# Performance work log

Measured on AMD Instinct MI355X. Metric: run time of the kernel, lower is better.

Reference implementation:

```python
import jax, jax.numpy as jnp
import numpy as np

N = 8192
E = 262144
D_IN = 256
D_OUT = 256
EPS = 1e-05


def setup_inputs() -> dict:
    key = jax.random.key(0)
    kx, ke0, ke1, kw = jax.random.split(key, 4)
    x = jax.random.normal(kx, (N, D_IN), dtype=jnp.float32)
    edge_index = jnp.stack([
        jax.random.randint(ke0, (E,), 0, N, dtype=jnp.int64),
        jax.random.randint(ke1, (E,), 0, N, dtype=jnp.int64),
    ], axis=0)
    # nn.Linear(in, out, bias=False): weight shape [out, in], kaiming-uniform-ish init
    bound = 1.0 / np.sqrt(D_IN)
    W = jax.random.uniform(kw, (D_OUT, D_IN), dtype=jnp.float32, minval=-bound, maxval=bound)
    return {"x": x, "edge_index": edge_index, "W": W}


def reference(x, edge_index, W):
    n = x.shape[0]
    # A_hat = I with edges set to 1 (set semantics; duplicates harmless)
    A_hat = jnp.eye(n, dtype=x.dtype).at[edge_index[0], edge_index[1]].set(1.0)
    # D_hat = diag(1/sqrt(rowsum + eps)); A_norm = D_hat @ A_hat @ D_hat
    d_inv = 1.0 / jnp.sqrt(A_hat.sum(axis=1) + EPS)  # [N]
    A_norm = d_inv[:, None] * A_hat * d_inv[None, :]  # [N, N]
    h = x @ W.T  # [N, D_OUT]
    return jax.nn.relu(A_norm @ h)
```

## Files before the change

kernel.cpp:

```cpp
#include <hip/hip_runtime.h>
#include <hip/hip_bf16.h>
#include <math.h>

#define N_NODES 8192
#define DIM 256
#define WPR 256
#define LSTRIDE 128

typedef __attribute__((ext_vector_type(8))) short bf16x8;
typedef __attribute__((ext_vector_type(4))) float f32x4;

__global__ __launch_bounds__(256) void init_all(const float* __restrict__ x,
                                                const float* __restrict__ W,
                                                unsigned* __restrict__ bitmap,
                                                __hip_bfloat16* __restrict__ xb,
                                                __hip_bfloat16* __restrict__ Wb) {
    unsigned tid = blockIdx.x * 256 + threadIdx.x;
    uint4 z = {0u, 0u, 0u, 0u};
    ((uint4*)bitmap)[tid] = z;
    const unsigned NX8 = N_NODES * DIM / 8;
    if (tid < NX8 + DIM * DIM / 8) {
        const float* src = x;
        __hip_bfloat16* dst = xb;
        size_t off = (size_t)tid * 8;
        if (tid >= NX8) { src = W; dst = Wb; off = (size_t)(tid - NX8) * 8; }
        float4 v0 = *(const float4*)(src + off);
        float4 v1 = *(const float4*)(src + off + 4);
        union { __hip_bfloat16 h[8]; uint4 u; } t;
        t.h[0] = __float2bfloat16(v0.x); t.h[1] = __float2bfloat16(v0.y);
        t.h[2] = __float2bfloat16(v0.z); t.h[3] = __float2bfloat16(v0.w);
        t.h[4] = __float2bfloat16(v1.x); t.h[5] = __float2bfloat16(v1.y);
        t.h[6] = __float2bfloat16(v1.z); t.h[7] = __float2bfloat16(v1.w);
        *(uint4*)(dst + off) = t.u;
    }
}

__global__ __launch_bounds__(256) void scatter_edges(const int* __restrict__ rows,
                                                     const int* __restrict__ cols,
                                                     unsigned* __restrict__ bitmap, int E) {
    int e = blockIdx.x * 256 + threadIdx.x;
    if (e >= E) return;
    int r = rows[e];
    int c = cols[e];
    atomicOr(&bitmap[(size_t)r * WPR + (c >> 5)], 1u << (c & 31));
}

__global__ __launch_bounds__(256) void dinv_and_list(const unsigned* __restrict__ bitmap,
                                                     float* __restrict__ dinv,
                                                     int* __restrict__ lens,
                                                     unsigned short* __restrict__ list) {
    int wave = threadIdx.x >> 6;
    int lane = threadIdx.x & 63;
    int row = blockIdx.x * 4 + wave;
    const uint4* base = (const uint4*)(bitmap + (size_t)row * WPR);
    uint4 w = base[lane];
    int c = __popc(w.x) + __popc(w.y) + __popc(w.z) + __popc(w.w);
    int dw = row >> 5;
    int diag = 0;
    if ((dw >> 2) == lane) {
        unsigned word = ((dw & 3) == 0) ? w.x : ((dw & 3) == 1) ? w.y : ((dw & 3) == 2) ? w.z : w.w;
        diag = (int)((word >> (row & 31)) & 1u);
    }
    unsigned long long db = __ballot(diag);
    int p = c;
#pragma unroll
    for (int off = 1; off < 64; off <<= 1) {
        int v = __shfl_up(p, off);
        if (lane >= off) p += v;
    }
    int total = __shfl(p, 63);
    unsigned short* lp = list + (size_t)row * LSTRIDE + (p - c);
    int k = 0;
    unsigned ws[4] = {w.x, w.y, w.z, w.w};
#pragma unroll
    for (int q = 0; q < 4; q++) {
        unsigned ww = ws[q];
        int bc = lane * 128 + q * 32;
        while (ww) {
            int b = __builtin_ctz(ww);
            ww &= ww - 1;
            lp[k++] = (unsigned short)(bc + b);
        }
    }
    int len = total + (db == 0ull ? 1 : 0);
    if (db == 0ull && lane == 0) list[(size_t)row * LSTRIDE + total] = (unsigned short)row;
    if (lane == 0) {
        lens[row] = len;
        dinv[row] = 1.0f / sqrtf((float)len + 1e-5f);
    }
}

__global__ __launch_bounds__(256) void gemm_mfma(const short* __restrict__ xb,
                                                 const short* __restrict__ Wb,
                                                 const float* __restrict__ dinv,
                                                 __hip_bfloat16* __restrict__ g) {
    int wave = threadIdx.x >> 6;
    int lane = threadIdx.x & 63;
    int bm = blockIdx.x * 64 + wave * 16;
    int bn = blockIdx.y * 64;
    int quad = lane >> 4;
    int l16 = lane & 15;
    f32x4 acc[4] = {};
    const short* arow = xb + (size_t)(bm + l16) * DIM + quad * 8;
#pragma unroll
    for (int k0 = 0; k0 < DIM; k0 += 32) {
        bf16x8 a = *(const bf16x8*)(arow + k0);
#pragma unroll
        for (int s = 0; s < 4; s++) {
            bf16x8 b = *(const bf16x8*)(Wb + (size_t)(bn + s * 16 + l16) * DIM + k0 + quad * 8);
            acc[s] = __builtin_amdgcn_mfma_f32_16x16x32_bf16(a, b, acc[s], 0, 0, 0);
        }
    }
#pragma unroll
    for (int r = 0; r < 4; r++) {
        int m = bm + quad * 4 + r;
        float s0 = dinv[m];
#pragma unroll
        for (int s = 0; s < 4; s++)
            g[(size_t)m * DIM + bn + s * 16 + l16] = __float2bfloat16(s0 * acc[s][r]);
    }
}

__global__ __launch_bounds__(128) void aggregate(const unsigned short* __restrict__ list,
                                                 const int* __restrict__ lens,
                                                 const uint4* __restrict__ g4,
                                                 const float* __restrict__ dinv,
                                                 float* __restrict__ out) {
    __shared__ unsigned short snbr[LSTRIDE];
    __shared__ float part[4][DIM];
    int row = blockIdx.x;
    int tid = threadIdx.x;
    snbr[tid] = list[(size_t)row * LSTRIDE + tid];
    int len = lens[row];
    __syncthreads();
    int gq = tid >> 5, l = tid & 31;
    float a0 = 0.f, a1 = 0.f, a2 = 0.f, a3 = 0.f, a4 = 0.f, a5 = 0.f, a6 = 0.f, a7 = 0.f;
    float b0 = 0.f, b1 = 0.f, b2 = 0.f, b3 = 0.f, b4 = 0.f, b5 = 0.f, b6 = 0.f, b7 = 0.f;
    int i = gq;
    for (; i + 4 < len; i += 8) {
        int n0 = snbr[i];
        int n1 = snbr[i + 4];
        uint4 u0 = g4[(size_t)n0 * 32 + l];
        uint4 u1 = g4[(size_t)n1 * 32 + l];
        a0 += __uint_as_float(u0.x << 16); a1 += __uint_as_float(u0.x & 0xffff0000u);
        a2 += __uint_as_float(u0.y << 16); a3 += __uint_as_float(u0.y & 0xffff0000u);
        a4 += __uint_as_float(u0.z << 16); a5 += __uint_as_float(u0.z & 0xffff0000u);
        a6 += __uint_as_float(u0.w << 16); a7 += __uint_as_float(u0.w & 0xffff0000u);
        b0 += __uint_as_float(u1.x << 16); b1 += __uint_as_float(u1.x & 0xffff0000u);
        b2 += __uint_as_float(u1.y << 16); b3 += __uint_as_float(u1.y & 0xffff0000u);
        b4 += __uint_as_float(u1.z << 16); b5 += __uint_as_float(u1.z & 0xffff0000u);
        b6 += __uint_as_float(u1.w << 16); b7 += __uint_as_float(u1.w & 0xffff0000u);
    }
    if (i < len) {
        int n0 = snbr[i];
        uint4 u0 = g4[(size_t)n0 * 32 + l];
        a0 += __uint_as_float(u0.x << 16); a1 += __uint_as_float(u0.x & 0xffff0000u);
        a2 += __uint_as_float(u0.y << 16); a3 += __uint_as_float(u0.y & 0xffff0000u);
        a4 += __uint_as_float(u0.z << 16); a5 += __uint_as_float(u0.z & 0xffff0000u);
        a6 += __uint_as_float(u0.w << 16); a7 += __uint_as_float(u0.w & 0xffff0000u);
    }
    float* pp = &part[gq][l * 8];
    pp[0] = a0 + b0; pp[1] = a1 + b1; pp[2] = a2 + b2; pp[3] = a3 + b3;
    pp[4] = a4 + b4; pp[5] = a5 + b5; pp[6] = a6 + b6; pp[7] = a7 + b7;
    __syncthreads();
    int f0 = tid * 2;
    float s = dinv[row];
    float r0 = (part[0][f0] + part[1][f0]) + (part[2][f0] + part[3][f0]);
    float r1 = (part[0][f0 + 1] + part[1][f0 + 1]) + (part[2][f0 + 1] + part[3][f0 + 1]);
    float2 o;
    o.x = fmaxf(s * r0, 0.f);
    o.y = fmaxf(s * r1, 0.f);
    *(float2*)(out + (size_t)row * DIM + f0) = o;
}

extern "C" void kernel_launch(void* const* d_in, const int* in_sizes, int n_in,
                              void* d_out, int out_size, void* d_ws, size_t ws_size,
                              hipStream_t stream) {
    const float* x = (const float*)d_in[0];
    const int* ei = (const int*)d_in[1];
    const float* W = (const float*)d_in[2];
    float* out = (float*)d_out;
    int E = in_sizes[1] / 2;

    unsigned char* ws = (unsigned char*)d_ws;
    size_t off = 0;
    unsigned* bitmap = (unsigned*)(ws + off); off += (size_t)N_NODES * WPR * 4;
    float* dinv = (float*)(ws + off);         off += (size_t)N_NODES * 4;
    int* lens = (int*)(ws + off);             off += (size_t)N_NODES * 4;
    unsigned short* list = (unsigned short*)(ws + off); off += (size_t)N_NODES * LSTRIDE * 2;
    __hip_bfloat16* xb = (__hip_bfloat16*)(ws + off); off += (size_t)N_NODES * DIM * 2;
    __hip_bfloat16* Wb = (__hip_bfloat16*)(ws + off); off += (size_t)DIM * DIM * 2;
    __hip_bfloat16* g = (__hip_bfloat16*)(ws + off);  off += (size_t)N_NODES * DIM * 2;

    init_all<<<2048, 256, 0, stream>>>(x, W, bitmap, xb, Wb);
    scatter_edges<<<(E + 255) / 256, 256, 0, stream>>>(ei, ei + E, bitmap, E);
    dinv_and_list<<<N_NODES / 4, 256, 0, stream>>>(bitmap, dinv, lens, list);
    dim3 ggrid(N_NODES / 64, DIM / 64);
    gemm_mfma<<<ggrid, 256, 0, stream>>>((const short*)xb, (const short*)Wb, dinv, g);
    aggregate<<<N_NODES, 128, 0, stream>>>(list, lens, (const uint4*)g, dinv, out);
}
```

Before: 103.3 us.

## Fuse GCN pipeline into one cooperative persistent kernel with grid syncs

Replaces the five separate launches with a single cooperative kernel that runs zeroing, scatter+convert, GEMM and degree/list construction concurrently (split across half the blocks), then aggregation, separated by grid.sync. GEMM no longer depends on dinv: the source-side normalization moves into aggregation as a per-neighbor FMA with dinv gathered into shared memory. The aim is to remove launch gaps and overlap the GEMM with list building. In exchange it adds grid-wide barrier costs and a grid capped at occupancy, and it keeps a multi-kernel fallback.

```diff
diff --git a/kernel.cpp b/kernel.cpp
--- a/kernel.cpp
+++ b/kernel.cpp
@@ -1,6 +1,9 @@
 #include <hip/hip_runtime.h>
 #include <hip/hip_bf16.h>
+#include <hip/hip_cooperative_groups.h>
 #include <math.h>
+
+namespace cg = cooperative_groups;
 
 #define N_NODES 8192
 #define DIM 256
@@ -10,167 +13,253 @@
 typedef __attribute__((ext_vector_type(8))) short bf16x8;
 typedef __attribute__((ext_vector_type(4))) float f32x4;
 
-__global__ __launch_bounds__(256) void init_all(const float* __restrict__ x,
-                                                const float* __restrict__ W,
-                                                unsigned* __restrict__ bitmap,
-                                                __hip_bfloat16* __restrict__ xb,
-                                                __hip_bfloat16* __restrict__ Wb) {
-    unsigned tid = blockIdx.x * 256 + threadIdx.x;
+
+__device__ __forceinline__ void phase_zero(unsigned* __restrict__ bitmap, int gtid, int nth) {
+    const int NB4 = N_NODES * WPR / 4;
     uint4 z = {0u, 0u, 0u, 0u};
-    ((uint4*)bitmap)[tid] = z;
-    const unsigned NX8 = N_NODES * DIM / 8;
-    if (tid < NX8 + DIM * DIM / 8) {
+    for (int i = gtid; i < NB4; i += nth) ((uint4*)bitmap)[i] = z;
+}
+
+__device__ __forceinline__ void phase_scatter(const int* __restrict__ rows, const int* __restrict__ cols,
+                                              unsigned* __restrict__ bitmap, int E, int gtid, int nth) {
+    for (int e = gtid; e < E; e += nth) {
+        int r = rows[e];
+        int c = cols[e];
+        atomicOr(&bitmap[(size_t)r * WPR + (c >> 5)], 1u << (c & 31));
+    }
+}
+
+__device__ __forceinline__ void phase_convert(const float* __restrict__ x, const float* __restrict__ W,
+                                              __hip_bfloat16* __restrict__ xb, __hip_bfloat16* __restrict__ Wb,
+                                              int gtid, int nth) {
+    const int NX8 = N_NODES * DIM / 8;
+    const int NTOT = NX8 + DIM * DIM / 8;
+    for (int t = gtid; t < NTOT; t += nth) {
         const float* src = x;
         __hip_bfloat16* dst = xb;
-        size_t off = (size_t)tid * 8;
-        if (tid >= NX8) { src = W; dst = Wb; off = (size_t)(tid - NX8) * 8; }
+        size_t off = (size_t)t * 8;
+        if (t >= NX8) { src = W; dst = Wb; off = (size_t)(t - NX8) * 8; }
         float4 v0 = *(const float4*)(src + off);
         float4 v1 = *(const float4*)(src + off + 4);
-        union { __hip_bfloat16 h[8]; uint4 u; } t;
-        t.h[0] = __float2bfloat16(v0.x); t.h[1] = __float2bfloat16(v0.y);
-        t.h[2] = __float2bfloat16(v0.z); t.h[3] = __float2bfloat16(v0.w);
-        t.h[4] = __float2bfloat16(v1.x); t.h[5] = __float2bfloat16(v1.y);
-        t.h[6] = __float2bfloat16(v1.z); t.h[7] = __float2bfloat16(v1.w);
-        *(uint4*)(dst + off) = t.u;
-    }
-}
-
-__global__ __launch_bounds__(256) void scatter_edges(const int* __restrict__ rows,
-                                                     const int* __restrict__ cols,
-                                                     unsigned* __restrict__ bitmap, int E) {
-    int e = blockIdx.x * 256 + threadIdx.x;
-    if (e >= E) return;
-    int r = rows[e];
-    int c = cols[e];
-    atomicOr(&bitmap[(size_t)r * WPR + (c >> 5)], 1u << (c & 31));
-}
-
-__global__ __launch_bounds__(256) void dinv_and_list(const unsigned* __restrict__ bitmap,
-                                                     float* __restrict__ dinv,
-                                                     int* __restrict__ lens,
-                                                     unsigned short* __restrict__ list) {
-    int wave = threadIdx.x >> 6;
-    int lane = threadIdx.x & 63;
-    int row = blockIdx.x * 4 + wave;
-    const uint4* base = (const uint4*)(bitmap + (size_t)row * WPR);
-    uint4 w = base[lane];
-    int c = __popc(w.x) + __popc(w.y) + __popc(w.z) + __popc(w.w);
-    int dw = row >> 5;
-    int diag = 0;
-    if ((dw >> 2) == lane) {
-        unsigned word = ((dw & 3) == 0) ? w.x : ((dw & 3) == 1) ? w.y : ((dw & 3) == 2) ? w.z : w.w;
-        diag = (int)((word >> (row & 31)) & 1u);
-    }
-    unsigned long long db = __ballot(diag);
-    int p = c;
-#pragma unroll
-    for (int off = 1; off < 64; off <<= 1) {
-        int v = __shfl_up(p, off);
-        if (lane >= off) p += v;
-    }
-    int total = __shfl(p, 63);
-    unsigned short* lp = list + (size_t)row * LSTRIDE + (p - c);
-    int k = 0;
-    unsigned ws[4] = {w.x, w.y, w.z, w.w};
-#pragma unroll
-    for (int q = 0; q < 4; q++) {
-        unsigned ww = ws[q];
-        int bc = lane * 128 + q * 32;
-        while (ww) {
-            int b = __builtin_ctz(ww);
-            ww &= ww - 1;
-            lp[k++] = (unsigned short)(bc + b);
-        }
-    }
-    int len = total + (db == 0ull ? 1 : 0);
-    if (db == 0ull && lane == 0) list[(size_t)row * LSTRIDE + total] = (unsigned short)row;
-    if (lane == 0) {
-        lens[row] = len;
-        dinv[row] = 1.0f / sqrtf((float)len + 1e-5f);
-    }
-}
-
-__global__ __launch_bounds__(256) void gemm_mfma(const short* __restrict__ xb,
-                                                 const short* __restrict__ Wb,
-                                                 const float* __restrict__ dinv,
-                                                 __hip_bfloat16* __restrict__ g) {
-    int wave = threadIdx.x >> 6;
-    int lane = threadIdx.x & 63;
-    int bm = blockIdx.x * 64 + wave * 16;
-    int bn = blockIdx.y * 64;
-    int quad = lane >> 4;
-    int l16 = lane & 15;
-    f32x4 acc[4] = {};
-    const short* arow = xb + (size_t)(bm + l16) * DIM + quad * 8;
-#pragma unroll
-    for (int k0 = 0; k0 < DIM; k0 += 32) {
-        bf16x8 a = *(const bf16x8*)(arow + k0);
-#pragma unroll
-        for (int s = 0; s < 4; s++) {
-            bf16x8 b = *(const bf16x8*)(Wb + (size_t)(bn + s * 16 + l16) * DIM + k0 + quad * 8);
-            acc[s] = __builtin_amdgcn_mfma_f32_16x16x32_bf16(a, b, acc[s], 0, 0, 0);
-        }
-    }
-#pragma unroll
-    for (int r = 0; r < 4; r++) {
-        int m = bm + quad * 4 + r;
-        float s0 = dinv[m];
-#pragma unroll
-        for (int s = 0; s < 4; s++)
-            g[(size_t)m * DIM + bn + s * 16 + l16] = __float2bfloat16(s0 * acc[s][r]);
-    }
-}
-
-__global__ __launch_bounds__(128) void aggregate(const unsigned short* __restrict__ list,
-                                                 const int* __restrict__ lens,
-                                                 const uint4* __restrict__ g4,
-                                                 const float* __restrict__ dinv,
-                                                 float* __restrict__ out) {
-    __shared__ unsigned short snbr[LSTRIDE];
-    __shared__ float part[4][DIM];
-    int row = blockIdx.x;
-    int tid = threadIdx.x;
-    snbr[tid] = list[(size_t)row * LSTRIDE + tid];
-    int len = lens[row];
-    __syncthreads();
-    int gq = tid >> 5, l = tid & 31;
-    float a0 = 0.f, a1 = 0.f, a2 = 0.f, a3 = 0.f, a4 = 0.f, a5 = 0.f, a6 = 0.f, a7 = 0.f;
-    float b0 = 0.f, b1 = 0.f, b2 = 0.f, b3 = 0.f, b4 = 0.f, b5 = 0.f, b6 = 0.f, b7 = 0.f;
-    int i = gq;
-    for (; i + 4 < len; i += 8) {
-        int n0 = snbr[i];
-        int n1 = snbr[i + 4];
-        uint4 u0 = g4[(size_t)n0 * 32 + l];
-        uint4 u1 = g4[(size_t)n1 * 32 + l];
-        a0 += __uint_as_float(u0.x << 16); a1 += __uint_as_float(u0.x & 0xffff0000u);
-        a2 += __uint_as_float(u0.y << 16); a3 += __uint_as_float(u0.y & 0xffff0000u);
-        a4 += __uint_as_float(u0.z << 16); a5 += __uint_as_float(u0.z & 0xffff0000u);
-        a6 += __uint_as_float(u0.w << 16); a7 += __uint_as_float(u0.w & 0xffff0000u);
-        b0 += __uint_as_float(u1.x << 16); b1 += __uint_as_float(u1.x & 0xffff0000u);
-        b2 += __uint_as_float(u1.y << 16); b3 += __uint_as_float(u1.y & 0xffff0000u);
-        b4 += __uint_as_float(u1.z << 16); b5 += __uint_as_float(u1.z & 0xffff0000u);
-        b6 += __uint_as_float(u1.w << 16); b7 += __uint_as_float(u1.w & 0xffff0000u);
-    }
-    if (i < len) {
-        int n0 = snbr[i];
-        uint4 u0 = g4[(size_t)n0 * 32 + l];
-        a0 += __uint_as_float(u0.x << 16); a1 += __uint_as_float(u0.x & 0xffff0000u);
-        a2 += __uint_as_float(u0.y << 16); a3 += __uint_as_float(u0.y & 0xffff0000u);
-        a4 += __uint_as_float(u0.z << 16); a5 += __uint_as_float(u0.z & 0xffff0000u);
-        a6 += __uint_as_float(u0.w << 16); a7 += __uint_as_float(u0.w & 0xffff0000u);
-    }
-    float* pp = &part[gq][l * 8];
-    pp[0] = a0 + b0; pp[1] = a1 + b1; pp[2] = a2 + b2; pp[3] = a3 + b3;
-    pp[4] = a4 + b4; pp[5] = a5 + b5; pp[6] = a6 + b6; pp[7] = a7 + b7;
-    __syncthreads();
-    int f0 = tid * 2;
-    float s = dinv[row];
-    float r0 = (part[0][f0] + part[1][f0]) + (part[2][f0] + part[3][f0]);
-    float r1 = (part[0][f0 + 1] + part[1][f0 + 1]) + (part[2][f0 + 1] + part[3][f0 + 1]);
-    float2 o;
-    o.x = fmaxf(s * r0, 0.f);
-    o.y = fmaxf(s * r1, 0.f);
-    *(float2*)(out + (size_t)row * DIM + f0) = o;
+        union { __hip_bfloat16 h[8]; uint4 u; } c;
+        c.h[0] = __float2bfloat16(v0.x); c.h[1] = __float2bfloat16(v0.y);
+        c.h[2] = __float2bfloat16(v0.z); c.h[3] = __float2bfloat16(v0.w);
+        c.h[4] = __float2bfloat16(v1.x); c.h[5] = __float2bfloat16(v1.y);
+        c.h[6] = __float2bfloat16(v1.z); c.h[7] = __float2bfloat16(v1.w);
+        *(uint4*)(dst + off) = c.u;
+    }
+}
+
+__device__ __forceinline__ void phase_gemm(const short* __restrict__ xb, const short* __restrict__ Wb,
+                                           __hip_bfloat16* __restrict__ g, int bid, int nblk, int tid) {
+    int wave = tid >> 6, lane = tid & 63;
+    int quad = lane >> 4, l16 = lane & 15;
+    for (int t = bid; t < 512; t += nblk) {
+        int bm = (t & 127) * 64 + wave * 16;
+        int bn = (t >> 7) * 64;
+        f32x4 acc[4] = {};
+        const short* arow = xb + (size_t)(bm + l16) * DIM + quad * 8;
+#pragma unroll
+        for (int k0 = 0; k0 < DIM; k0 += 32) {
+            bf16x8 a = *(const bf16x8*)(arow + k0);
+#pragma unroll
+            for (int s = 0; s < 4; s++) {
+                bf16x8 b = *(const bf16x8*)(Wb + (size_t)(bn + s * 16 + l16) * DIM + k0 + quad * 8);
+                acc[s] = __builtin_amdgcn_mfma_f32_16x16x32_bf16(a, b, acc[s], 0, 0, 0);
+            }
+        }
+#pragma unroll
+        for (int r = 0; r < 4; r++) {
+            int m = bm + quad * 4 + r;
+#pragma unroll
+            for (int s = 0; s < 4; s++)
+                g[(size_t)m * DIM + bn + s * 16 + l16] = __float2bfloat16(acc[s][r]);
+        }
+    }
+}
+
+__device__ __forceinline__ void phase_dinvlist(const unsigned* __restrict__ bitmap, float* __restrict__ dinv,
+                                               int* __restrict__ lens, unsigned short* __restrict__ list,
+                                               int bid, int nblk, int tid) {
+    int wave = tid >> 6, lane = tid & 63;
+    int nw = nblk * 4;
+    for (int row = bid * 4 + wave; row < N_NODES; row += nw) {
+        const uint4* base = (const uint4*)(bitmap + (size_t)row * WPR);
+        uint4 w = base[lane];
+        int c = __popc(w.x) + __popc(w.y) + __popc(w.z) + __popc(w.w);
+        int dw = row >> 5;
+        int diag = 0;
+        if ((dw >> 2) == lane) {
+            unsigned word = ((dw & 3) == 0) ? w.x : ((dw & 3) == 1) ? w.y : ((dw & 3) == 2) ? w.z : w.w;
+            diag = (int)((word >> (row & 31)) & 1u);
+        }
+        unsigned long long db = __ballot(diag);
+        int p = c;
+#pragma unroll
+        for (int off = 1; off < 64; off <<= 1) {
+            int v = __shfl_up(p, off);
+            if (lane >= off) p += v;
+        }
+        int total = __shfl(p, 63);
+        unsigned short* lp = list + (size_t)row * LSTRIDE + (p - c);
+        int k = 0;
+        unsigned wsv[4] = {w.x, w.y, w.z, w.w};
+#pragma unroll
+        for (int q = 0; q < 4; q++) {
+            unsigned ww = wsv[q];
+            int bc = lane * 128 + q * 32;
+            while (ww) {
+                int b = __builtin_ctz(ww);
+                ww &= ww - 1;
+                lp[k++] = (unsigned short)(bc + b);
+            }
+        }
+        int len = total + (db == 0ull ? 1 : 0);
+        if (db == 0ull && lane == 0) list[(size_t)row * LSTRIDE + total] = (unsigned short)row;
+        if (lane == 0) {
+            lens[row] = len;
+            dinv[row] = 1.0f / sqrtf((float)len + 1e-5f);
+        }
+    }
+}
+
+__device__ __forceinline__ void phase_aggregate(const unsigned short* __restrict__ list,
+                                                const int* __restrict__ lens,
+                                                const float* __restrict__ dinv,
+                                                const uint4* __restrict__ g4,
+                                                float* __restrict__ out, int bid, int nblk, int tid) {
+    __shared__ unsigned short snbr[2][LSTRIDE];
+    __shared__ float sdj[2][LSTRIDE];
+    __shared__ float part[2][4][DIM];
+    int team = tid >> 7;
+    int ttid = tid & 127;
+    int gq = ttid >> 5, l = ttid & 31;
+    int nteams = nblk * 2;
+    for (int base = 0; base < N_NODES; base += nteams) {
+        int row = base + bid * 2 + team;
+        bool active = row < N_NODES;
+        int len = 0;
+        if (active) {
+            unsigned short nb = list[(size_t)row * LSTRIDE + ttid];
+            snbr[team][ttid] = nb;
+            sdj[team][ttid] = dinv[nb & (N_NODES - 1)];
+            len = lens[row];
+        }
+        __syncthreads();
+        if (active) {
+            float a0 = 0.f, a1 = 0.f, a2 = 0.f, a3 = 0.f, a4 = 0.f, a5 = 0.f, a6 = 0.f, a7 = 0.f;
+            float b0 = 0.f, b1 = 0.f, b2 = 0.f, b3 = 0.f, b4 = 0.f, b5 = 0.f, b6 = 0.f, b7 = 0.f;
+            int i = gq;
+            for (; i + 4 < len; i += 8) {
+                int n0 = snbr[team][i];
+                int n1 = snbr[team][i + 4];
+                float d0 = sdj[team][i];
+                float d1 = sdj[team][i + 4];
+                uint4 u0 = g4[(size_t)n0 * 32 + l];
+                uint4 u1 = g4[(size_t)n1 * 32 + l];
+                a0 = fmaf(d0, __uint_as_float(u0.x << 16), a0);
+                a1 = fmaf(d0, __uint_as_float(u0.x & 0xffff0000u), a1);
+                a2 = fmaf(d0, __uint_as_float(u0.y << 16), a2);
+                a3 = fmaf(d0, __uint_as_float(u0.y & 0xffff0000u), a3);
+                a4 = fmaf(d0, __uint_as_float(u0.z << 16), a4);
+                a5 = fmaf(d0, __uint_as_float(u0.z & 0xffff0000u), a5);
+                a6 = fmaf(d0, __uint_as_float(u0.w << 16), a6);
+                a7 = fmaf(d0, __uint_as_float(u0.w & 0xffff0000u), a7);
+                b0 = fmaf(d1, __uint_as_float(u1.x << 16), b0);
+                b1 = fmaf(d1, __uint_as_float(u1.x & 0xffff0000u), b1);
+                b2 = fmaf(d1, __uint_as_float(u1.y << 16), b2);
+                b3 = fmaf(d1, __uint_as_float(u1.y & 0xffff0000u), b3);
+                b4 = fmaf(d1, __uint_as_float(u1.z << 16), b4);
+                b5 = fmaf(d1, __uint_as_float(u1.z & 0xffff0000u), b5);
+                b6 = fmaf(d1, __uint_as_float(u1.w << 16), b6);
+                b7 = fmaf(d1, __uint_as_float(u1.w & 0xffff0000u), b7);
+            }
+            if (i < len) {
+                int n0 = snbr[team][i];
+                float d0 = sdj[team][i];
+                uint4 u0 = g4[(size_t)n0 * 32 + l];
+                a0 = fmaf(d0, __uint_as_float(u0.x << 16), a0);
+                a1 = fmaf(d0, __uint_as_float(u0.x & 0xffff0000u), a1);
+                a2 = fmaf(d0, __uint_as_float(u0.y << 16), a2);
+                a3 = fmaf(d0, __uint_as_float(u0.y & 0xffff0000u), a3);
+                a4 = fmaf(d0, __uint_as_float(u0.z << 16), a4);
+                a5 = fmaf(d0, __uint_as_float(u0.z & 0xffff0000u), a5);
+                a6 = fmaf(d0, __uint_as_float(u0.w << 16), a6);
+                a7 = fmaf(d0, __uint_as_float(u0.w & 0xffff0000u), a7);
+            }
+            float* pp = &part[team][gq][l * 8];
+            pp[0] = a0 + b0; pp[1] = a1 + b1; pp[2] = a2 + b2; pp[3] = a3 + b3;
+            pp[4] = a4 + b4; pp[5] = a5 + b5; pp[6] = a6 + b6; pp[7] = a7 + b7;
+        }
+        __syncthreads();
+        if (active) {
+            int f0 = ttid * 2;
+            float s = dinv[row];
+            float r0 = (part[team][0][f0] + part[team][1][f0]) + (part[team][2][f0] + part[team][3][f0]);
+            float r1 = (part[team][0][f0 + 1] + part[team][1][f0 + 1]) + (part[team][2][f0 + 1] + part[team][3][f0 + 1]);
+            float2 o;
+            o.x = fmaxf(s * r0, 0.f);
+            o.y = fmaxf(s * r1, 0.f);
+            *(float2*)(out + (size_t)row * DIM + f0) = o;
+        }
+        __syncthreads();
+    }
+}
+
+__global__ __launch_bounds__(256, 4) void fused_gcn(const float* __restrict__ x,
+                                                    const int* __restrict__ ei,
+                                                    const float* __restrict__ W,
+                                                    float* __restrict__ out,
+                                                    unsigned* __restrict__ bitmap,
+                                                    float* __restrict__ dinv,
+                                                    int* __restrict__ lens,
+                                                    unsigned short* __restrict__ list,
+                                                    __hip_bfloat16* __restrict__ xb,
+                                                    __hip_bfloat16* __restrict__ Wb,
+                                                    __hip_bfloat16* __restrict__ g,
+                                                    int E) {
+    cg::grid_group grid = cg::this_grid();
+    int tid = threadIdx.x, bid = blockIdx.x, nblk = gridDim.x;
+    int gtid = bid * 256 + tid, nth = nblk * 256;
+
+    phase_zero(bitmap, gtid, nth);
+    grid.sync();
+
+    phase_scatter(ei, ei + E, bitmap, E, gtid, nth);
+    phase_convert(x, W, xb, Wb, gtid, nth);
+    grid.sync();
+
+    int half = nblk >> 1;
+    if (bid < half) phase_gemm((const short*)xb, (const short*)Wb, g, bid, half, tid);
+    else            phase_dinvlist(bitmap, dinv, lens, list, bid - half, nblk - half, tid);
+    grid.sync();
+
+    phase_aggregate(list, lens, dinv, (const uint4*)g, out, bid, nblk, tid);
+}
+
+__global__ __launch_bounds__(256) void k_init(const float* __restrict__ x, const float* __restrict__ W,
+                                              unsigned* __restrict__ bitmap,
+                                              __hip_bfloat16* __restrict__ xb, __hip_bfloat16* __restrict__ Wb) {
+    int gtid = blockIdx.x * 256 + threadIdx.x, nth = gridDim.x * 256;
+    phase_zero(bitmap, gtid, nth);
+    phase_convert(x, W, xb, Wb, gtid, nth);
+}
+__global__ __launch_bounds__(256) void k_scatter(const int* __restrict__ ei, unsigned* __restrict__ bitmap, int E) {
+    int gtid = blockIdx.x * 256 + threadIdx.x, nth = gridDim.x * 256;
+    phase_scatter(ei, ei + E, bitmap, E, gtid, nth);
+}
+__global__ __launch_bounds__(256) void k_dinvlist(const unsigned* __restrict__ bitmap, float* __restrict__ dinv,
+                                                  int* __restrict__ lens, unsigned short* __restrict__ list) {
+    phase_dinvlist(bitmap, dinv, lens, list, blockIdx.x, gridDim.x, threadIdx.x);
+}
+__global__ __launch_bounds__(256) void k_gemm(const short* __restrict__ xb, const short* __restrict__ Wb,
+                                              __hip_bfloat16* __restrict__ g) {
+    phase_gemm(xb, Wb, g, blockIdx.x, gridDim.x, threadIdx.x);
+}
+__global__ __launch_bounds__(256) void k_aggregate(const unsigned short* __restrict__ list, const int* __restrict__ lens,
+                                                   const float* __restrict__ dinv, const uint4* __restrict__ g4,
+                                                   float* __restrict__ out) {
+    phase_aggregate(list, lens, dinv, g4, out, blockIdx.x, gridDim.x, threadIdx.x);
 }
 
 extern "C" void kernel_launch(void* const* d_in, const int* in_sizes, int n_in,
@@ -192,10 +281,22 @@
     __hip_bfloat16* Wb = (__hip_bfloat16*)(ws + off); off += (size_t)DIM * DIM * 2;
     __hip_bfloat16* g = (__hip_bfloat16*)(ws + off);  off += (size_t)N_NODES * DIM * 2;
 
-    init_all<<<2048, 256, 0, stream>>>(x, W, bitmap, xb, Wb);
-    scatter_edges<<<(E + 255) / 256, 256, 0, stream>>>(ei, ei + E, bitmap, E);
-    dinv_and_list<<<N_NODES / 4, 256, 0, stream>>>(bitmap, dinv, lens, list);
-    dim3 ggrid(N_NODES / 64, DIM / 64);
-    gemm_mfma<<<ggrid, 256, 0, stream>>>((const short*)xb, (const short*)Wb, dinv, g);
-    aggregate<<<N_NODES, 128, 0, stream>>>(list, lens, (const uint4*)g, dinv, out);
-}
+    int nblk = 1024;
+    int maxPerCU = 0;
+    if (hipOccupancyMaxActiveBlocksPerMultiprocessor(&maxPerCU, fused_gcn, 256, 0) == hipSuccess && maxPerCU >= 1) {
+        int cap = maxPerCU * 256;
+        if (cap < nblk) nblk = cap;
+    }
+
+    const uint4* g4c = (const uint4*)g;
+    void* args[12] = {(void*)&x, (void*)&ei, (void*)&W, (void*)&out, (void*)&bitmap, (void*)&dinv,
+                      (void*)&lens, (void*)&list, (void*)&xb, (void*)&Wb, (void*)&g, (void*)&E};
+    hipError_t rc = hipLaunchCooperativeKernel(fused_gcn, dim3(nblk), dim3(256), args, 0, stream);
+    if (rc != hipSuccess) {
+        k_init<<<2048, 256, 0, stream>>>(x, W, bitmap, xb, Wb);
+        k_scatter<<<1024, 256, 0, stream>>>(ei, bitmap, E);
+        k_dinvlist<<<2048, 256, 0, stream>>>(bitmap, dinv, lens, list);
+        k_gemm<<<512, 256, 0, stream>>>((const short*)xb, (const short*)Wb, g);
+        k_aggregate<<<4096, 256, 0, stream>>>(list, lens, dinv, g4c, out);
+    }
+}
```

Measured after the change: 399.3 us. 287% more time.

## Replace dense bitmap with atomic adjacency lists, dedup in GEMM kernel

Applied to the files above, without the earlier changes.

Drops the 8 MB dense adjacency bitmap, its zeroing and the full-bitmap scan. Edges now go straight into per-row neighbor lists via atomicAdd on a length counter, fused into the conversion kernel. Deduplication and degree computation run in a shared-memory bitmap inside the GEMM launch as extra blocks. Because the per-column normalization is no longer known when the GEMM runs, it moves into the aggregation loop as an FMA with a gathered dinv. This cuts five launches to three plus a memset, but assumes no row exceeds 128 raw edges (overflow entries are dropped) and needs an extra dinv gather per neighbor.

```diff
diff --git a/kernel.cpp b/kernel.cpp
--- a/kernel.cpp
+++ b/kernel.cpp
@@ -10,127 +10,120 @@
 typedef __attribute__((ext_vector_type(8))) short bf16x8;
 typedef __attribute__((ext_vector_type(4))) float f32x4;
 
-__global__ __launch_bounds__(256) void init_all(const float* __restrict__ x,
-                                                const float* __restrict__ W,
-                                                unsigned* __restrict__ bitmap,
-                                                __hip_bfloat16* __restrict__ xb,
-                                                __hip_bfloat16* __restrict__ Wb) {
-    unsigned tid = blockIdx.x * 256 + threadIdx.x;
-    uint4 z = {0u, 0u, 0u, 0u};
-    ((uint4*)bitmap)[tid] = z;
-    const unsigned NX8 = N_NODES * DIM / 8;
-    if (tid < NX8 + DIM * DIM / 8) {
+__global__ __launch_bounds__(256) void k1_convert_scatter(
+        const float* __restrict__ x, const float* __restrict__ W, const int* __restrict__ ei,
+        __hip_bfloat16* __restrict__ xb, __hip_bfloat16* __restrict__ Wb,
+        unsigned short* __restrict__ list, int* __restrict__ lens, int E) {
+    const int CONV_BLOCKS = (N_NODES * DIM / 8 + DIM * DIM / 8) / 256;
+    if ((int)blockIdx.x < CONV_BLOCKS) {
+        int t = blockIdx.x * 256 + threadIdx.x;
+        const int NX8 = N_NODES * DIM / 8;
         const float* src = x;
         __hip_bfloat16* dst = xb;
-        size_t off = (size_t)tid * 8;
-        if (tid >= NX8) { src = W; dst = Wb; off = (size_t)(tid - NX8) * 8; }
+        size_t off = (size_t)t * 8;
+        if (t >= NX8) { src = W; dst = Wb; off = (size_t)(t - NX8) * 8; }
         float4 v0 = *(const float4*)(src + off);
         float4 v1 = *(const float4*)(src + off + 4);
-        union { __hip_bfloat16 h[8]; uint4 u; } t;
-        t.h[0] = __float2bfloat16(v0.x); t.h[1] = __float2bfloat16(v0.y);
-        t.h[2] = __float2bfloat16(v0.z); t.h[3] = __float2bfloat16(v0.w);
-        t.h[4] = __float2bfloat16(v1.x); t.h[5] = __float2bfloat16(v1.y);
-        t.h[6] = __float2bfloat16(v1.z); t.h[7] = __float2bfloat16(v1.w);
-        *(uint4*)(dst + off) = t.u;
-    }
-}
-
-__global__ __launch_bounds__(256) void scatter_edges(const int* __restrict__ rows,
-                                                     const int* __restrict__ cols,
-                                                     unsigned* __restrict__ bitmap, int E) {
-    int e = blockIdx.x * 256 + threadIdx.x;
-    if (e >= E) return;
-    int r = rows[e];
-    int c = cols[e];
-    atomicOr(&bitmap[(size_t)r * WPR + (c >> 5)], 1u << (c & 31));
-}
-
-__global__ __launch_bounds__(256) void dinv_and_list(const unsigned* __restrict__ bitmap,
-                                                     float* __restrict__ dinv,
-                                                     int* __restrict__ lens,
-                                                     unsigned short* __restrict__ list) {
-    int wave = threadIdx.x >> 6;
-    int lane = threadIdx.x & 63;
-    int row = blockIdx.x * 4 + wave;
-    const uint4* base = (const uint4*)(bitmap + (size_t)row * WPR);
-    uint4 w = base[lane];
-    int c = __popc(w.x) + __popc(w.y) + __popc(w.z) + __popc(w.w);
-    int dw = row >> 5;
-    int diag = 0;
-    if ((dw >> 2) == lane) {
-        unsigned word = ((dw & 3) == 0) ? w.x : ((dw & 3) == 1) ? w.y : ((dw & 3) == 2) ? w.z : w.w;
-        diag = (int)((word >> (row & 31)) & 1u);
-    }
-    unsigned long long db = __ballot(diag);
-    int p = c;
-#pragma unroll
-    for (int off = 1; off < 64; off <<= 1) {
-        int v = __shfl_up(p, off);
-        if (lane >= off) p += v;
-    }
-    int total = __shfl(p, 63);
-    unsigned short* lp = list + (size_t)row * LSTRIDE + (p - c);
-    int k = 0;
-    unsigned ws[4] = {w.x, w.y, w.z, w.w};
-#pragma unroll
-    for (int q = 0; q < 4; q++) {
-        unsigned ww = ws[q];
-        int bc = lane * 128 + q * 32;
-        while (ww) {
-            int b = __builtin_ctz(ww);
-            ww &= ww - 1;
-            lp[k++] = (unsigned short)(bc + b);
-        }
-    }
-    int len = total + (db == 0ull ? 1 : 0);
-    if (db == 0ull && lane == 0) list[(size_t)row * LSTRIDE + total] = (unsigned short)row;
-    if (lane == 0) {
-        lens[row] = len;
-        dinv[row] = 1.0f / sqrtf((float)len + 1e-5f);
-    }
-}
-
-__global__ __launch_bounds__(256) void gemm_mfma(const short* __restrict__ xb,
-                                                 const short* __restrict__ Wb,
-                                                 const float* __restrict__ dinv,
-                                                 __hip_bfloat16* __restrict__ g) {
-    int wave = threadIdx.x >> 6;
-    int lane = threadIdx.x & 63;
-    int bm = blockIdx.x * 64 + wave * 16;
-    int bn = blockIdx.y * 64;
-    int quad = lane >> 4;
-    int l16 = lane & 15;
-    f32x4 acc[4] = {};
-    const short* arow = xb + (size_t)(bm + l16) * DIM + quad * 8;
-#pragma unroll
-    for (int k0 = 0; k0 < DIM; k0 += 32) {
-        bf16x8 a = *(const bf16x8*)(arow + k0);
-#pragma unroll
-        for (int s = 0; s < 4; s++) {
-            bf16x8 b = *(const bf16x8*)(Wb + (size_t)(bn + s * 16 + l16) * DIM + k0 + quad * 8);
-            acc[s] = __builtin_amdgcn_mfma_f32_16x16x32_bf16(a, b, acc[s], 0, 0, 0);
-        }
-    }
-#pragma unroll
-    for (int r = 0; r < 4; r++) {
-        int m = bm + quad * 4 + r;
-        float s0 = dinv[m];
-#pragma unroll
-        for (int s = 0; s < 4; s++)
-            g[(size_t)m * DIM + bn + s * 16 + l16] = __float2bfloat16(s0 * acc[s][r]);
-    }
-}
-
-__global__ __launch_bounds__(128) void aggregate(const unsigned short* __restrict__ list,
-                                                 const int* __restrict__ lens,
-                                                 const uint4* __restrict__ g4,
-                                                 const float* __restrict__ dinv,
-                                                 float* __restrict__ out) {
+        union { __hip_bfloat16 h[8]; uint4 u; } c;
+        c.h[0] = __float2bfloat16(v0.x); c.h[1] = __float2bfloat16(v0.y);
+        c.h[2] = __float2bfloat16(v0.z); c.h[3] = __float2bfloat16(v0.w);
+        c.h[4] = __float2bfloat16(v1.x); c.h[5] = __float2bfloat16(v1.y);
+        c.h[6] = __float2bfloat16(v1.z); c.h[7] = __float2bfloat16(v1.w);
+        *(uint4*)(dst + off) = c.u;
+    } else {
+        int sid = (blockIdx.x - CONV_BLOCKS) * 256 + threadIdx.x;
+        int snth = (gridDim.x - CONV_BLOCKS) * 256;
+        const int* rows = ei;
+        const int* cols = ei + E;
+        for (int e = sid; e < E; e += snth) {
+            int r = rows[e];
+            int c = cols[e];
+            int pos = atomicAdd(&lens[r], 1);
+            if (pos < LSTRIDE) list[(size_t)r * LSTRIDE + pos] = (unsigned short)c;
+        }
+    }
+}
+
+__global__ __launch_bounds__(256) void k2_gemm_dedup(
+        const short* __restrict__ xb, const short* __restrict__ Wb, __hip_bfloat16* __restrict__ g,
+        unsigned short* __restrict__ list, int* __restrict__ lens, float* __restrict__ dinv) {
+    __shared__ unsigned sbm[4][WPR];
+    if ((int)blockIdx.x < 512) {
+        int tid = threadIdx.x;
+        int wave = tid >> 6, lane = tid & 63;
+        int quad = lane >> 4, l16 = lane & 15;
+        int t = blockIdx.x;
+        int bm = (t & 127) * 64 + wave * 16;
+        int bn = (t >> 7) * 64;
+        f32x4 acc[4] = {};
+        const short* arow = xb + (size_t)(bm + l16) * DIM + quad * 8;
+#pragma unroll
+        for (int k0 = 0; k0 < DIM; k0 += 32) {
+            bf16x8 a = *(const bf16x8*)(arow + k0);
+#pragma unroll
+            for (int s = 0; s < 4; s++) {
+                bf16x8 b = *(const bf16x8*)(Wb + (size_t)(bn + s * 16 + l16) * DIM + k0 + quad * 8);
+                acc[s] = __builtin_amdgcn_mfma_f32_16x16x32_bf16(a, b, acc[s], 0, 0, 0);
+            }
+        }
+#pragma unroll
+        for (int r = 0; r < 4; r++) {
+            int m = bm + quad * 4 + r;
+#pragma unroll
+            for (int s = 0; s < 4; s++)
+                g[(size_t)m * DIM + bn + s * 16 + l16] = __float2bfloat16(acc[s][r]);
+        }
+    } else {
+        int bid = blockIdx.x - 512;
+        int wave = threadIdx.x >> 6, lane = threadIdx.x & 63;
+        for (int row = bid * 4 + wave; row < N_NODES; row += 512 * 4) {
+            uint4 z = {0u, 0u, 0u, 0u};
+            *(uint4*)&sbm[wave][lane * 4] = z;
+            unsigned short* lp = list + (size_t)row * LSTRIDE;
+            int raw = lens[row];
+            if (raw > LSTRIDE) raw = LSTRIDE;
+            int c0 = (lane < raw) ? (int)lp[lane] : -1;
+            int c1 = (64 + lane < raw) ? (int)lp[64 + lane] : -1;
+            int new0 = 0, new1 = 0;
+            if (c0 >= 0) {
+                unsigned old = atomicOr(&sbm[wave][c0 >> 5], 1u << (c0 & 31));
+                new0 = !((old >> (c0 & 31)) & 1u);
+            }
+            if (c1 >= 0) {
+                unsigned old = atomicOr(&sbm[wave][c1 >> 5], 1u << (c1 & 31));
+                new1 = !((old >> (c1 & 31)) & 1u);
+            }
+            unsigned long long m0 = __ballot(new0);
+            unsigned long long m1 = __ballot(new1);
+            unsigned long long below = (1ull << lane) - 1ull;
+            int kept0 = __popcll(m0);
+            int pos0 = __popcll(m0 & below);
+            int pos1 = kept0 + __popcll(m1 & below);
+            int total = kept0 + __popcll(m1);
+            int diag = (int)((sbm[wave][row >> 5] >> (row & 31)) & 1u);
+            if (new0) lp[pos0] = (unsigned short)c0;
+            if (new1) lp[pos1] = (unsigned short)c1;
+            if (!diag && lane == 0) lp[total] = (unsigned short)row;
+            if (lane == 0) {
+                int len = total + (diag ? 0 : 1);
+                lens[row] = len;
+                dinv[row] = 1.0f / sqrtf((float)len + 1e-5f);
+            }
+        }
+    }
+}
+
+__global__ __launch_bounds__(128) void k3_aggregate(
+        const unsigned short* __restrict__ list, const int* __restrict__ lens,
+        const float* __restrict__ dinv, const uint4* __restrict__ g4, float* __restrict__ out) {
     __shared__ unsigned short snbr[LSTRIDE];
+    __shared__ float sdj[LSTRIDE];
     __shared__ float part[4][DIM];
     int row = blockIdx.x;
     int tid = threadIdx.x;
-    snbr[tid] = list[(size_t)row * LSTRIDE + tid];
+    unsigned short nb = list[(size_t)row * LSTRIDE + tid];
+    snbr[tid] = nb;
+    sdj[tid] = dinv[nb & (N_NODES - 1)];
     int len = lens[row];
     __syncthreads();
     int gq = tid >> 5, l = tid & 31;
@@ -140,24 +133,39 @@
     for (; i + 4 < len; i += 8) {
         int n0 = snbr[i];
         int n1 = snbr[i + 4];
+        float d0 = sdj[i];
+        float d1 = sdj[i + 4];
         uint4 u0 = g4[(size_t)n0 * 32 + l];
         uint4 u1 = g4[(size_t)n1 * 32 + l];
-        a0 += __uint_as_float(u0.x << 16); a1 += __uint_as_float(u0.x & 0xffff0000u);
-        a2 += __uint_as_float(u0.y << 16); a3 += __uint_as_float(u0.y & 0xffff0000u);
-        a4 += __uint_as_float(u0.z << 16); a5 += __uint_as_float(u0.z & 0xffff0000u);
-        a6 += __uint_as_float(u0.w << 16); a7 += __uint_as_float(u0.w & 0xffff0000u);
-        b0 += __uint_as_float(u1.x << 16); b1 += __uint_as_float(u1.x & 0xffff0000u);
-        b2 += __uint_as_float(u1.y << 16); b3 += __uint_as_float(u1.y & 0xffff0000u);
-        b4 += __uint_as_float(u1.z << 16); b5 += __uint_as_float(u1.z & 0xffff0000u);
-        b6 += __uint_as_float(u1.w << 16); b7 += __uint_as_float(u1.w & 0xffff0000u);
+        a0 = fmaf(d0, __uint_as_float(u0.x << 16), a0);
+        a1 = fmaf(d0, __uint_as_float(u0.x & 0xffff0000u), a1);
+        a2 = fmaf(d0, __uint_as_float(u0.y << 16), a2);
+        a3 = fmaf(d0, __uint_as_float(u0.y & 0xffff0000u), a3);
+        a4 = fmaf(d0, __uint_as_float(u0.z << 16), a4);
+        a5 = fmaf(d0, __uint_as_float(u0.z & 0xffff0000u), a5);
+        a6 = fmaf(d0, __uint_as_float(u0.w << 16), a6);
+        a7 = fmaf(d0, __uint_as_float(u0.w & 0xffff0000u), a7);
+        b0 = fmaf(d1, __uint_as_float(u1.x << 16), b0);
+        b1 = fmaf(d1, __uint_as_float(u1.x & 0xffff0000u), b1);
+        b2 = fmaf(d1, __uint_as_float(u1.y << 16), b2);
+        b3 = fmaf(d1, __uint_as_float(u1.y & 0xffff0000u), b3);
+        b4 = fmaf(d1, __uint_as_float(u1.z << 16), b4);
+        b5 = fmaf(d1, __uint_as_float(u1.z & 0xffff0000u), b5);
+        b6 = fmaf(d1, __uint_as_float(u1.w << 16), b6);
+        b7 = fmaf(d1, __uint_as_float(u1.w & 0xffff0000u), b7);
     }
     if (i < len) {
         int n0 = snbr[i];
+        float d0 = sdj[i];
         uint4 u0 = g4[(size_t)n0 * 32 + l];
-        a0 += __uint_as_float(u0.x << 16); a1 += __uint_as_float(u0.x & 0xffff0000u);
-        a2 += __uint_as_float(u0.y << 16); a3 += __uint_as_float(u0.y & 0xffff0000u);
-        a4 += __uint_as_float(u0.z << 16); a5 += __uint_as_float(u0.z & 0xffff0000u);
-        a6 += __uint_as_float(u0.w << 16); a7 += __uint_as_float(u0.w & 0xffff0000u);
+        a0 = fmaf(d0, __uint_as_float(u0.x << 16), a0);
+        a1 = fmaf(d0, __uint_as_float(u0.x & 0xffff0000u), a1);
+        a2 = fmaf(d0, __uint_as_float(u0.y << 16), a2);
+        a3 = fmaf(d0, __uint_as_float(u0.y & 0xffff0000u), a3);
+        a4 = fmaf(d0, __uint_as_float(u0.z << 16), a4);
+        a5 = fmaf(d0, __uint_as_float(u0.z & 0xffff0000u), a5);
+        a6 = fmaf(d0, __uint_as_float(u0.w << 16), a6);
+        a7 = fmaf(d0, __uint_as_float(u0.w & 0xffff0000u), a7);
     }
     float* pp = &part[gq][l * 8];
     pp[0] = a0 + b0; pp[1] = a1 + b1; pp[2] = a2 + b2; pp[3] = a3 + b3;
@@ -184,18 +192,16 @@
 
     unsigned char* ws = (unsigned char*)d_ws;
     size_t off = 0;
-    unsigned* bitmap = (unsigned*)(ws + off); off += (size_t)N_NODES * WPR * 4;
-    float* dinv = (float*)(ws + off);         off += (size_t)N_NODES * 4;
-    int* lens = (int*)(ws + off);             off += (size_t)N_NODES * 4;
+    int* lens = (int*)(ws + off);                       off += (size_t)N_NODES * 4;
+    float* dinv = (float*)(ws + off);                   off += (size_t)N_NODES * 4;
     unsigned short* list = (unsigned short*)(ws + off); off += (size_t)N_NODES * LSTRIDE * 2;
-    __hip_bfloat16* xb = (__hip_bfloat16*)(ws + off); off += (size_t)N_NODES * DIM * 2;
-    __hip_bfloat16* Wb = (__hip_bfloat16*)(ws + off); off += (size_t)DIM * DIM * 2;
-    __hip_bfloat16* g = (__hip_bfloat16*)(ws + off);  off += (size_t)N_NODES * DIM * 2;
-
-    init_all<<<2048, 256, 0, stream>>>(x, W, bitmap, xb, Wb);
-    scatter_edges<<<(E + 255) / 256, 256, 0, stream>>>(ei, ei + E, bitmap, E);
-    dinv_and_list<<<N_NODES / 4, 256, 0, stream>>>(bitmap, dinv, lens, list);
-    dim3 ggrid(N_NODES / 64, DIM / 64);
-    gemm_mfma<<<ggrid, 256, 0, stream>>>((const short*)xb, (const short*)Wb, dinv, g);
-    aggregate<<<N_NODES, 128, 0, stream>>>(list, lens, (const uint4*)g, dinv, out);
-}
+    __hip_bfloat16* xb = (__hip_bfloat16*)(ws + off);   off += (size_t)N_NODES * DIM * 2;
+    __hip_bfloat16* Wb = (__hip_bfloat16*)(ws + off);   off += (size_t)DIM * DIM * 2;
+    __hip_bfloat16* g = (__hip_bfloat16*)(ws + off);    off += (size_t)N_NODES * DIM * 2;
+
+    hipMemsetAsync(lens, 0, (size_t)N_NODES * 4, stream);
+    const int CONV_BLOCKS = (N_NODES * DIM / 8 + DIM * DIM / 8) / 256;
+    k1_convert_scatter<<<CONV_BLOCKS + 512, 256, 0, stream>>>(x, W, ei, xb, Wb, list, lens, E);
+    k2_gemm_dedup<<<1024, 256, 0, stream>>>((const short*)xb, (const short*)Wb, g, list, lens, dinv);
+    k3_aggregate<<<N_NODES, 128, 0, stream>>>(list, lens, dinv, (const uint4*)g, out);
+}
```

Result: no change. 103.2 us (-0.1%).
